# Optimization experiments

Measured on AMD Instinct MI355X. Metric: run time of the kernel, lower is better.

## Reference

```python
import jax, jax.numpy as jnp
import numpy as np

B, S, T, H, VS, VE = 32, 128, 128, 512, 8000, 8000


def _lstm_scan(x_proj, W_hh, bias, h0, c0):
    # x_proj: [L, B, 4H] precomputed input projections; gate order i,f,g,o (PyTorch)
    def step(carry, xp):
        h, c = carry
        gates = xp + h @ W_hh.T + bias  # [B, 4H]
        i, f, g, o = jnp.split(gates, 4, axis=-1)
        c = jax.nn.sigmoid(f) * c + jax.nn.sigmoid(i) * jnp.tanh(g)
        h = jax.nn.sigmoid(o) * jnp.tanh(c)
        return (h, c), h
    (h, c), hs = jax.lax.scan(step, (h0, c0), x_proj)
    return hs, h, c


def setup_inputs() -> dict:
    key = jax.random.key(0)
    ks = jax.random.split(key, 16)
    sc_h = 1.0 / np.sqrt(H)
    u = lambda k, shape: jax.random.uniform(k, shape, jnp.float32, -sc_h, sc_h)
    return {
        "input_batch": jax.random.randint(ks[0], (B, S), 0, VS),
        "output_batch": jax.random.randint(ks[1], (B, T), 0, VE),
        "Wa": u(ks[2], (H, H)), "ba": u(ks[3], (H,)),
        "W1": u(ks[4], (H, 2 * H)), "b1": u(ks[5], (H,)),
        "W2": u(ks[6], (VE, H)), "b2": u(ks[7], (VE,)),
        "We_ih": u(ks[8], (4 * H, VS)), "We_hh": u(ks[9], (4 * H, H)),
        "be_ih": u(ks[10], (4 * H,)), "be_hh": u(ks[11], (4 * H,)),
        "Wd_ih": u(ks[12], (4 * H, VE)), "Wd_hh": u(ks[13], (4 * H, H)),
        "bd_ih": u(ks[14], (4 * H,)), "bd_hh": u(ks[15], (4 * H,)),
    }


def reference(input_batch, output_batch, Wa, ba, W1, b1, W2, b2,
              We_ih, We_hh, be_ih, be_hh, Wd_ih, Wd_hh, bd_ih, bd_hh):
    src = input_batch.T  # [S, B]
    tgt = output_batch.T  # [T, B]
    # one_hot(tok) @ W_ih.T  ==  W_ih.T[tok]  (gather instead of dense one-hot GEMM)
    enc_xp = jnp.take(We_ih.T, src, axis=0)  # [S, B, 4H]
    dec_xp = jnp.take(Wd_ih.T, tgt, axis=0)  # [T, B, 4H]
    h0 = jnp.zeros((B, H), jnp.float32)
    c0 = jnp.zeros((B, H), jnp.float32)
    enc_outputs, h, c = _lstm_scan(enc_xp, We_hh, be_ih + be_hh, h0, c0)  # [S,B,H]
    proj_enc = enc_outputs @ Wa.T + ba  # attn(enc_outputs): [S, B, H]
    dec_bias = bd_ih + bd_hh

    def dec_step(carry, xp):
        h, c = carry
        gates = xp + h @ Wd_hh.T + dec_bias
        i, f, g, o = jnp.split(gates, 4, axis=-1)
        c = jax.nn.sigmoid(f) * c + jax.nn.sigmoid(i) * jnp.tanh(g)
        h = jax.nn.sigmoid(o) * jnp.tanh(c)  # [B, H] == dec_output
        scores = jnp.einsum('sbh,bh->bs', proj_enc, h)  # [B, S]
        w = jax.nn.softmax(scores, axis=1)
        context = jnp.einsum('bs,sbh->bh', w, enc_outputs)  # [B, H]
        hid = jnp.tanh(jnp.concatenate([h, context], axis=1) @ W1.T + b1)
        logits = hid @ W2.T + b2  # [B, VE]
        return (h, c), logits

    _, model = jax.lax.scan(dec_step, (h, c), dec_xp)  # [T, B, VE]
    return jax.nn.softmax(model.transpose(1, 0, 2), axis=2)  # [B, T, VE]
```

## Files before the change

### kernel.cpp

```cpp
#include <hip/hip_runtime.h>
#include <hip/hip_cooperative_groups.h>

#define NB 32
#define NS 128
#define NT 128
#define NH 512
#define NVS 8000
#define NVE 8000

typedef float fx4 __attribute__((ext_vector_type(4)));

__device__ __forceinline__ float sigm(float x) { return 1.0f / (1.0f + expf(-x)); }

__device__ __forceinline__ fx4 load_cg(const float* p) {
  fx4 v;
  asm volatile("global_load_dwordx4 %0, %1, off sc0 sc1" : "=v"(v) : "v"(p));
  return v;
}
__device__ __forceinline__ void store_cg(float* p, fx4 v) {
  asm volatile("global_store_dwordx4 %0, %1, off sc0 sc1" :: "v"(p), "v"(v) : "memory");
}

__global__ __launch_bounds__(256) void scan_kernel(
    const int* __restrict__ in_tok, const int* __restrict__ out_tok,
    const float* __restrict__ We_ih, const float* __restrict__ We_hh,
    const float* __restrict__ be_ih, const float* __restrict__ be_hh,
    const float* __restrict__ Wd_ih, const float* __restrict__ Wd_hh,
    const float* __restrict__ bd_ih, const float* __restrict__ bd_hh,
    float* __restrict__ h_buf,
    float* __restrict__ enc_out,
    float* __restrict__ dec_h,
    int* __restrict__ flags)
{
  __shared__ float W_lds[16][520];
  __shared__ float h_lds[16 * 516];
  __shared__ float gbuf[16][16];
  __shared__ float c_buf[4][16];
  __shared__ float hstage[16][4];

  const int tid = threadIdx.x;
  const int g   = blockIdx.x;
  const int bg  = g & 1;
  const int mg  = g >> 1;
  const int r   = tid >> 4;
  const int bl  = tid & 15;
  const int b   = bg * 16 + bl;
  const int q   = r >> 2;
  const int i   = r & 3;
  const int j   = q * NH + mg * 4 + i;

  const float bias_e = be_ih[j] + be_hh[j];
  const float bias_d = bd_ih[j] + bd_hh[j];
  const float* Wcol_e = We_ih + (size_t)j * NVS;
  const float* Wcol_d = Wd_ih + (size_t)j * NVE;

  if (tid < 64) c_buf[tid >> 4][tid & 15] = 0.0f;

  {
    const float* Wg = We_hh;
    for (int u = tid; u < 2048; u += 256) {
      const int rr = u >> 7;
      const int k4 = (u & 127) << 2;
      const int jj = (rr >> 2) * NH + mg * 4 + (rr & 3);
      *(float4*)&W_lds[rr][k4] = *(const float4*)(Wg + (size_t)jj * NH + k4);
    }
  }
  __syncthreads();

  for (int s = 0; s < NS + NT; ++s) {
    const bool enc = (s < NS);
    if (s == NS) {
      const float* Wg = Wd_hh;
      for (int u = tid; u < 2048; u += 256) {
        const int rr = u >> 7;
        const int k4 = (u & 127) << 2;
        const int jj = (rr >> 2) * NH + mg * 4 + (rr & 3);
        *(float4*)&W_lds[rr][k4] = *(const float4*)(Wg + (size_t)jj * NH + k4);
      }
      __syncthreads();
    }
    const int st  = enc ? s : s - NS;
    const int tok = enc ? in_tok[b * NS + st] : out_tok[b * NT + st];
    const float xp = enc ? Wcol_e[tok] : Wcol_d[tok];
    const float bias = enc ? bias_e : bias_d;
    const float* Wrow = &W_lds[r][0];

    float acc = 0.0f;
    if (s > 0) {
      if (tid < 128) {
        const int idx = (tid << 1) | bg;
        while (__hip_atomic_load(&flags[idx], __ATOMIC_RELAXED,
                                 __HIP_MEMORY_SCOPE_AGENT) < s)
          __builtin_amdgcn_s_sleep(1);
      }
      __syncthreads();
      const float* hsrc = h_buf + ((s - 1) & 1) * (NB * NH) + bg * 16 * NH;
      fx4 tmp[8];
      #pragma unroll
      for (int it = 0; it < 8; ++it)
        tmp[it] = load_cg(hsrc + ((tid + (it << 8)) << 2));
      asm volatile("s_waitcnt vmcnt(0)" ::: "memory");
      __builtin_amdgcn_sched_barrier(0);
      #pragma unroll
      for (int it = 0; it < 8; ++it) {
        const int u = tid + (it << 8);
        const int bb = u >> 7;
        const int kk = (u & 127) << 2;
        *(fx4*)&h_lds[bb * 516 + kk] = tmp[it];
      }
      __syncthreads();
      const float* hrow = &h_lds[bl * 516];
      #pragma unroll 8
      for (int k = 0; k < NH; k += 4) {
        const float4 hv = *(const float4*)(hrow + k);
        const float4 wv = *(const float4*)(Wrow + k);
        acc += hv.x * wv.x + hv.y * wv.y + hv.z * wv.z + hv.w * wv.w;
      }
    }
    gbuf[r][bl] = acc + xp + bias;
    __syncthreads();

    if (tid < 64) {
      const int ii = tid >> 4;
      const int bb = tid & 15;
      const float gi = gbuf[ii][bb];
      const float gf = gbuf[4 + ii][bb];
      const float gg = gbuf[8 + ii][bb];
      const float go = gbuf[12 + ii][bb];
      const float co = c_buf[ii][bb];
      const float cn = sigm(gf) * co + sigm(gi) * tanhf(gg);
      const float hn = sigm(go) * tanhf(cn);
      c_buf[ii][bb] = cn;
      hstage[bb][ii] = hn;
    }
    __syncthreads();
    if (tid < 16) {
      const fx4 hv = *(const fx4*)&hstage[tid][0];
      const int bglob = bg * 16 + tid;
      store_cg(h_buf + (s & 1) * (NB * NH) + bglob * NH + mg * 4, hv);
      float* dst = enc ? (enc_out + ((size_t)st * NB + bglob) * NH + mg * 4)
                       : (dec_h  + ((size_t)st * NB + bglob) * NH + mg * 4);
      *(fx4*)dst = hv;
    }
    asm volatile("s_waitcnt vmcnt(0)" ::: "memory");
    __syncthreads();
    if (tid == 0)
      __hip_atomic_store(&flags[g], s + 1, __ATOMIC_RELAXED,
                         __HIP_MEMORY_SCOPE_AGENT);
  }
}

template<int TRANSB, int CSWAP, int ACT>
__global__ __launch_bounds__(256) void gemm64(
    const float* __restrict__ A, const float* __restrict__ Bm,
    float* __restrict__ C, const float* __restrict__ bias,
    const float* __restrict__ A2, int ksplit,
    int M, int N, int K, int lda, int ldb, int ldc,
    long batchA, long batchB, long batchC)
{
  __shared__ float As[16][68];
  __shared__ float Bs[16][68];
  const int z = blockIdx.z;
  A += (long)z * batchA;
  if (A2 != nullptr) A2 += (long)z * batchA;
  Bm += (long)z * batchB;
  C  += (long)z * batchC;
  const int m0 = blockIdx.y << 6;
  const int n0 = blockIdx.x << 6;
  const int tid = threadIdx.x;
  const int tx = tid & 15;
  const int ty = tid >> 4;
  float acc[4][4] = {};

  for (int k0 = 0; k0 < K; k0 += 16) {
    {
      const int mrow = tid >> 2;
      const int kcq = (tid & 3) << 2;
      const float* base = A;
      int keff = k0;
      if (A2 != nullptr && k0 >= ksplit) { base = A2; keff = k0 - ksplit; }
      const float4 v = *(const float4*)(base + (long)(m0 + mrow) * lda + keff + kcq);
      As[kcq + 0][mrow] = v.x; As[kcq + 1][mrow] = v.y;
      As[kcq + 2][mrow] = v.z; As[kcq + 3][mrow] = v.w;
    }
    if (TRANSB == 0) {
      const int nrow = tid >> 2;
      const int kcq = (tid & 3) << 2;
      const float4 v = *(const float4*)(Bm + (long)(n0 + nrow) * ldb + k0 + kcq);
      Bs[kcq + 0][nrow] = v.x; Bs[kcq + 1][nrow] = v.y;
      Bs[kcq + 2][nrow] = v.z; Bs[kcq + 3][nrow] = v.w;
    } else {
      const int krow = tid >> 4;
      const int nc = (tid & 15) << 2;
      const float4 v = *(const float4*)(Bm + (long)(k0 + krow) * ldb + n0 + nc);
      *(float4*)&Bs[krow][nc] = v;
    }
    __syncthreads();
    #pragma unroll
    for (int kk = 0; kk < 16; ++kk) {
      const float4 a4 = *(const float4*)&As[kk][ty << 2];
      const float4 b4 = *(const float4*)&Bs[kk][tx << 2];
      const float a[4]  = {a4.x, a4.y, a4.z, a4.w};
      const float bv[4] = {b4.x, b4.y, b4.z, b4.w};
      #pragma unroll
      for (int ii = 0; ii < 4; ++ii)
        #pragma unroll
        for (int jj = 0; jj < 4; ++jj)
          acc[ii][jj] = fmaf(a[ii], bv[jj], acc[ii][jj]);
    }
    __syncthreads();
  }

  const int n = n0 + (tx << 2);
  float4 bb4 = {0.f, 0.f, 0.f, 0.f};
  if (bias) { bb4.x = bias[n]; bb4.y = bias[n + 1]; bb4.z = bias[n + 2]; bb4.w = bias[n + 3]; }
  #pragma unroll
  for (int ii = 0; ii < 4; ++ii) {
    const int mrow = m0 + (ty << 2) + ii;
    float4 o;
    o.x = acc[ii][0] + bb4.x; o.y = acc[ii][1] + bb4.y;
    o.z = acc[ii][2] + bb4.z; o.w = acc[ii][3] + bb4.w;
    if (ACT == 1) { o.x = tanhf(o.x); o.y = tanhf(o.y); o.z = tanhf(o.z); o.w = tanhf(o.w); }
    long orow = mrow;
    if (CSWAP) orow = (long)(mrow & (NB - 1)) * NT + (mrow >> 5);
    *(float4*)(C + orow * (long)ldc + n) = o;
  }
}

template<int CSWAP, int ACT>
__global__ __launch_bounds__(256) void gemm128(
    const float* __restrict__ A, const float* __restrict__ Bm,
    float* __restrict__ C, const float* __restrict__ bias,
    const float* __restrict__ A2, int ksplit,
    int M, int N, int K, int lda, int ldb, int ldc)
{
  __shared__ float As[16][132];
  __shared__ float Bs[16][68];
  const int m0 = blockIdx.y << 7;
  const int n0 = blockIdx.x << 6;
  const int tid = threadIdx.x;
  const int tx = tid & 15;
  const int ty = tid >> 4;
  float acc[8][4] = {};

  for (int k0 = 0; k0 < K; k0 += 16) {
    {
      const int mrow = tid >> 1;
      const int kq = (tid & 1) << 3;
      const float* base = A;
      int keff = k0;
      if (A2 != nullptr && k0 >= ksplit) { base = A2; keff = k0 - ksplit; }
      const float* p = base + (long)(m0 + mrow) * lda + keff + kq;
      const float4 v0 = *(const float4*)(p);
      const float4 v1 = *(const float4*)(p + 4);
      As[kq + 0][mrow] = v0.x; As[kq + 1][mrow] = v0.y;
      As[kq + 2][mrow] = v0.z; As[kq + 3][mrow] = v0.w;
      As[kq + 4][mrow] = v1.x; As[kq + 5][mrow] = v1.y;
      As[kq + 6][mrow] = v1.z; As[kq + 7][mrow] = v1.w;
    }
    {
      const int nrow = tid >> 2;
      const int kq = (tid & 3) << 2;
      const float4 v = *(const float4*)(Bm + (long)(n0 + nrow) * ldb + k0 + kq);
      Bs[kq + 0][nrow] = v.x; Bs[kq + 1][nrow] = v.y;
      Bs[kq + 2][nrow] = v.z; Bs[kq + 3][nrow] = v.w;
    }
    __syncthreads();
    #pragma unroll
    for (int kk = 0; kk < 16; ++kk) {
      const fx4 b4 = *(const fx4*)&Bs[kk][tx << 2];
      const fx4 a0 = *(const fx4*)&As[kk][ty << 3];
      const fx4 a1 = *(const fx4*)&As[kk][(ty << 3) + 4];
      #pragma unroll
      for (int ii = 0; ii < 4; ++ii) {
        #pragma unroll
        for (int jj = 0; jj < 4; ++jj) {
          acc[ii][jj]     = fmaf(a0[ii], b4[jj], acc[ii][jj]);
          acc[ii + 4][jj] = fmaf(a1[ii], b4[jj], acc[ii + 4][jj]);
        }
      }
    }
    __syncthreads();
  }

  const int n = n0 + (tx << 2);
  float4 bb4 = {0.f, 0.f, 0.f, 0.f};
  if (bias) { bb4.x = bias[n]; bb4.y = bias[n + 1]; bb4.z = bias[n + 2]; bb4.w = bias[n + 3]; }
  #pragma unroll
  for (int ii = 0; ii < 8; ++ii) {
    const int mrow = m0 + (ty << 3) + ii;
    float4 o;
    o.x = acc[ii][0] + bb4.x; o.y = acc[ii][1] + bb4.y;
    o.z = acc[ii][2] + bb4.z; o.w = acc[ii][3] + bb4.w;
    if (ACT == 1) { o.x = tanhf(o.x); o.y = tanhf(o.y); o.z = tanhf(o.z); o.w = tanhf(o.w); }
    long orow = mrow;
    if (CSWAP) orow = (long)(mrow & (NB - 1)) * NT + (mrow >> 5);
    *(float4*)(C + orow * (long)ldc + n) = o;
  }
}

__global__ __launch_bounds__(128) void softmax_s(float* __restrict__ sc) {
  const long row = blockIdx.x;
  float* p = sc + row * NS;
  const float x = p[threadIdx.x];
  float mx = x;
  for (int o = 32; o; o >>= 1) mx = fmaxf(mx, __shfl_xor(mx, o));
  __shared__ float r0[2], r1[2];
  const int w = threadIdx.x >> 6;
  if ((threadIdx.x & 63) == 0) r0[w] = mx;
  __syncthreads();
  mx = fmaxf(r0[0], r0[1]);
  const float e = expf(x - mx);
  float sum = e;
  for (int o = 32; o; o >>= 1) sum += __shfl_xor(sum, o);
  if ((threadIdx.x & 63) == 0) r1[w] = sum;
  __syncthreads();
  sum = r1[0] + r1[1];
  p[threadIdx.x] = e / sum;
}

__global__ __launch_bounds__(256) void softmax_v(float* __restrict__ out) {
  const long row = blockIdx.x;
  float* p = out + row * NVE;
  float v[32];
  float mx = -1e30f;
  #pragma unroll
  for (int it = 0; it < 32; ++it) {
    const int idx = (it << 8) + threadIdx.x;
    v[it] = (idx < NVE) ? p[idx] : -1e30f;
    mx = fmaxf(mx, v[it]);
  }
  for (int o = 32; o; o >>= 1) mx = fmaxf(mx, __shfl_xor(mx, o));
  __shared__ float red[4], red2[4];
  const int w = threadIdx.x >> 6;
  if ((threadIdx.x & 63) == 0) red[w] = mx;
  __syncthreads();
  mx = fmaxf(fmaxf(red[0], red[1]), fmaxf(red[2], red[3]));
  float sum = 0.0f;
  #pragma unroll
  for (int it = 0; it < 32; ++it) {
    const int idx = (it << 8) + threadIdx.x;
    if (idx < NVE) { v[it] = expf(v[it] - mx); sum += v[it]; }
  }
  for (int o = 32; o; o >>= 1) sum += __shfl_xor(sum, o);
  if ((threadIdx.x & 63) == 0) red2[w] = sum;
  __syncthreads();
  sum = red2[0] + red2[1] + red2[2] + red2[3];
  const float inv = 1.0f / sum;
  #pragma unroll
  for (int it = 0; it < 32; ++it) {
    const int idx = (it << 8) + threadIdx.x;
    if (idx < NVE) p[idx] = v[it] * inv;
  }
}

extern "C" void kernel_launch(void* const* d_in, const int* in_sizes, int n_in,
                              void* d_out, int out_size, void* d_ws, size_t ws_size,
                              hipStream_t stream) {
  const int*   in_tok = (const int*)d_in[0];
  const int*   out_tok = (const int*)d_in[1];
  const float* Wa    = (const float*)d_in[2];
  const float* ba    = (const float*)d_in[3];
  const float* W1    = (const float*)d_in[4];
  const float* b1    = (const float*)d_in[5];
  const float* W2    = (const float*)d_in[6];
  const float* b2    = (const float*)d_in[7];
  const float* We_ih = (const float*)d_in[8];
  const float* We_hh = (const float*)d_in[9];
  const float* be_ih = (const float*)d_in[10];
  const float* be_hh = (const float*)d_in[11];
  const float* Wd_ih = (const float*)d_in[12];
  const float* Wd_hh = (const float*)d_in[13];
  const float* bd_ih = (const float*)d_in[14];
  const float* bd_hh = (const float*)d_in[15];

  float* ws      = (float*)d_ws;
  float* h_buf   = ws;
  float* enc_out = ws + 32768;
  float* dec_h   = ws + 2129920;
  float* proj    = ws + 4227072;
  float* scores  = ws + 6324224;
  float* ctx     = ws + 6848512;
  float* hid     = ws + 8945664;
  int*   flags   = (int*)(ws + 11042816);
  float* out     = (float*)d_out;

  (void)hipMemsetAsync((void*)flags, 0, 256 * sizeof(int), stream);

  {
    void* args[14];
    args[0] = (void*)&in_tok; args[1] = (void*)&out_tok;
    args[2] = (void*)&We_ih;  args[3] = (void*)&We_hh;
    args[4] = (void*)&be_ih;  args[5] = (void*)&be_hh;
    args[6] = (void*)&Wd_ih;  args[7] = (void*)&Wd_hh;
    args[8] = (void*)&bd_ih;  args[9] = (void*)&bd_hh;
    args[10] = (void*)&h_buf; args[11] = (void*)&enc_out; args[12] = (void*)&dec_h;
    args[13] = (void*)&flags;
    (void)hipLaunchCooperativeKernel((void*)scan_kernel, dim3(256), dim3(256), args, 0, stream);
  }

  gemm128<0,0><<<dim3(8,32,1), 256, 0, stream>>>(
      enc_out, Wa, proj, ba, nullptr, 1 << 30,
      4096, 512, 512, 512, 512, 512);

  gemm64<0,0,0><<<dim3(2,2,NB), 256, 0, stream>>>(
      dec_h, proj, scores, nullptr, nullptr, 1 << 30,
      NT, NS, NH, NB * NH, NB * NH, NB * NS,
      (long)NH, (long)NH, (long)NS);

  softmax_s<<<dim3(NT * NB), 128, 0, stream>>>(scores);

  gemm64<1,0,0><<<dim3(8,2,NB), 256, 0, stream>>>(
      scores, enc_out, ctx, nullptr, nullptr, 1 << 30,
      NT, NH, NS, NB * NS, NB * NH, NB * NH,
      (long)NS, (long)NH, (long)NH);

  gemm128<0,1><<<dim3(8,32,1), 256, 0, stream>>>(
      dec_h, W1, hid, b1, ctx, 512,
      4096, 512, 1024, 512, 1024, 512);

  gemm128<1,0><<<dim3(125,32,1), 256, 0, stream>>>(
      hid, W2, out, b2, nullptr, 1 << 30,
      4096, NVE, 512, 512, 512, NVE);

  softmax_v<<<dim3(NB * NT), 256, 0, stream>>>(out);
}
```

Measured before the change: 2.240 ms.

## Decentralize scan flag polling per thread and use taller tile GEMM for vocab projection

In the recurrent scan kernel, each thread now polls only the producer flag for the slice of h it loads. This replaces the block-wide poll-then-barrier. The h-publish path uses wave shuffles instead of an LDS staging buffer, and the flag is set as soon as the h_buf store completes, before the enc_out/dec_h store, which shortens the serial critical path per timestep. Separately, the output vocab GEMM switches to a new 256x64-tile kernel to raise per-thread register reuse, at the cost of more registers and fewer blocks.

Measured after the change: 2.915 ms. 30.1% more time.

```diff
diff --git a/kernel.cpp b/kernel.cpp
--- a/kernel.cpp
+++ b/kernel.cpp
@@ -36,7 +36,6 @@
   __shared__ float h_lds[16 * 516];
   __shared__ float gbuf[16][16];
   __shared__ float c_buf[4][16];
-  __shared__ float hstage[16][4];
 
   const int tid = threadIdx.x;
   const int g   = blockIdx.x;
@@ -49,6 +48,10 @@
   const int i   = r & 3;
   const int j   = q * NH + mg * 4 + i;
 
+  const int gp  = tid >> 1;
+  const int hb  = tid & 1;
+  const int pflag = gp * 2 + bg;
+
   const float bias_e = be_ih[j] + be_hh[j];
   const float bias_d = bd_ih[j] + bd_hh[j];
   const float* Wcol_e = We_ih + (size_t)j * NVS;
@@ -56,26 +59,22 @@
 
   if (tid < 64) c_buf[tid >> 4][tid & 15] = 0.0f;
 
-  {
-    const float* Wg = We_hh;
-    for (int u = tid; u < 2048; u += 256) {
-      const int rr = u >> 7;
-      const int k4 = (u & 127) << 2;
-      const int jj = (rr >> 2) * NH + mg * 4 + (rr & 3);
-      *(float4*)&W_lds[rr][k4] = *(const float4*)(Wg + (size_t)jj * NH + k4);
-    }
+  for (int u = tid; u < 2048; u += 256) {
+    const int rr = u >> 7;
+    const int k4 = (u & 127) << 2;
+    const int jj = (rr >> 2) * NH + mg * 4 + (rr & 3);
+    *(float4*)&W_lds[rr][k4] = *(const float4*)(We_hh + (size_t)jj * NH + k4);
   }
   __syncthreads();
 
   for (int s = 0; s < NS + NT; ++s) {
     const bool enc = (s < NS);
     if (s == NS) {
-      const float* Wg = Wd_hh;
       for (int u = tid; u < 2048; u += 256) {
         const int rr = u >> 7;
         const int k4 = (u & 127) << 2;
         const int jj = (rr >> 2) * NH + mg * 4 + (rr & 3);
-        *(float4*)&W_lds[rr][k4] = *(const float4*)(Wg + (size_t)jj * NH + k4);
+        *(float4*)&W_lds[rr][k4] = *(const float4*)(Wd_hh + (size_t)jj * NH + k4);
       }
       __syncthreads();
     }
@@ -87,27 +86,19 @@
 
     float acc = 0.0f;
     if (s > 0) {
-      if (tid < 128) {
-        const int idx = (tid << 1) | bg;
-        while (__hip_atomic_load(&flags[idx], __ATOMIC_RELAXED,
-                                 __HIP_MEMORY_SCOPE_AGENT) < s)
-          __builtin_amdgcn_s_sleep(1);
-      }
-      __syncthreads();
+      while (__hip_atomic_load(&flags[pflag], __ATOMIC_RELAXED,
+                               __HIP_MEMORY_SCOPE_AGENT) < s)
+        __builtin_amdgcn_s_sleep(1);
       const float* hsrc = h_buf + ((s - 1) & 1) * (NB * NH) + bg * 16 * NH;
-      fx4 tmp[8];
-      #pragma unroll
-      for (int it = 0; it < 8; ++it)
-        tmp[it] = load_cg(hsrc + ((tid + (it << 8)) << 2));
+      fx4 t[8];
+      #pragma unroll
+      for (int u = 0; u < 8; ++u)
+        t[u] = load_cg(hsrc + (hb * 8 + u) * NH + gp * 4);
       asm volatile("s_waitcnt vmcnt(0)" ::: "memory");
       __builtin_amdgcn_sched_barrier(0);
       #pragma unroll
-      for (int it = 0; it < 8; ++it) {
-        const int u = tid + (it << 8);
-        const int bb = u >> 7;
-        const int kk = (u & 127) << 2;
-        *(fx4*)&h_lds[bb * 516 + kk] = tmp[it];
-      }
+      for (int u = 0; u < 8; ++u)
+        *(fx4*)&h_lds[(hb * 8 + u) * 516 + gp * 4] = t[u];
       __syncthreads();
       const float* hrow = &h_lds[bl * 516];
       #pragma unroll 8
@@ -131,22 +122,27 @@
       const float cn = sigm(gf) * co + sigm(gi) * tanhf(gg);
       const float hn = sigm(go) * tanhf(cn);
       c_buf[ii][bb] = cn;
-      hstage[bb][ii] = hn;
-    }
-    __syncthreads();
-    if (tid < 16) {
-      const fx4 hv = *(const fx4*)&hstage[tid][0];
-      const int bglob = bg * 16 + tid;
-      store_cg(h_buf + (s & 1) * (NB * NH) + bglob * NH + mg * 4, hv);
-      float* dst = enc ? (enc_out + ((size_t)st * NB + bglob) * NH + mg * 4)
-                       : (dec_h  + ((size_t)st * NB + bglob) * NH + mg * 4);
-      *(fx4*)dst = hv;
-    }
-    asm volatile("s_waitcnt vmcnt(0)" ::: "memory");
-    __syncthreads();
-    if (tid == 0)
-      __hip_atomic_store(&flags[g], s + 1, __ATOMIC_RELAXED,
-                         __HIP_MEMORY_SCOPE_AGENT);
+      const int lb = tid & 15;
+      fx4 hv;
+      hv.x = __shfl(hn, lb);
+      hv.y = __shfl(hn, lb + 16);
+      hv.z = __shfl(hn, lb + 32);
+      hv.w = __shfl(hn, lb + 48);
+      if (tid < 16) {
+        const int bglob = bg * 16 + tid;
+        store_cg(h_buf + (s & 1) * (NB * NH) + bglob * NH + mg * 4, hv);
+      }
+      asm volatile("s_waitcnt vmcnt(0)" ::: "memory");
+      if (tid == 0)
+        __hip_atomic_store(&flags[g], s + 1, __ATOMIC_RELAXED,
+                           __HIP_MEMORY_SCOPE_AGENT);
+      if (tid < 16) {
+        const int bglob = bg * 16 + tid;
+        float* dst = enc ? (enc_out + ((size_t)st * NB + bglob) * NH + mg * 4)
+                         : (dec_h  + ((size_t)st * NB + bglob) * NH + mg * 4);
+        *(fx4*)dst = hv;
+      }
+    }
   }
 }
 
@@ -299,6 +295,71 @@
   }
 }
 
+template<int CSWAP, int ACT>
+__global__ __launch_bounds__(256) void gemm256(
+    const float* __restrict__ A, const float* __restrict__ Bm,
+    float* __restrict__ C, const float* __restrict__ bias,
+    int M, int N, int K, int lda, int ldb, int ldc)
+{
+  __shared__ float As[16][260];
+  __shared__ float Bs[16][68];
+  const int m0 = blockIdx.y << 8;
+  const int n0 = blockIdx.x << 6;
+  const int tid = threadIdx.x;
+  const int tx = tid & 15;
+  const int ty = tid >> 4;
+  float acc[16][4] = {};
+
+  for (int k0 = 0; k0 < K; k0 += 16) {
+    {
+      const float* p = A + (long)(m0 + tid) * lda + k0;
+      #pragma unroll
+      for (int u = 0; u < 4; ++u) {
+        const float4 v = *(const float4*)(p + (u << 2));
+        As[(u << 2) + 0][tid] = v.x; As[(u << 2) + 1][tid] = v.y;
+        As[(u << 2) + 2][tid] = v.z; As[(u << 2) + 3][tid] = v.w;
+      }
+    }
+    {
+      const int nrow = tid >> 2;
+      const int kq = (tid & 3) << 2;
+      const float4 v = *(const float4*)(Bm + (long)(n0 + nrow) * ldb + k0 + kq);
+      Bs[kq + 0][nrow] = v.x; Bs[kq + 1][nrow] = v.y;
+      Bs[kq + 2][nrow] = v.z; Bs[kq + 3][nrow] = v.w;
+    }
+    __syncthreads();
+    #pragma unroll
+    for (int kk = 0; kk < 16; ++kk) {
+      const fx4 b4 = *(const fx4*)&Bs[kk][tx << 2];
+      #pragma unroll
+      for (int gq = 0; gq < 4; ++gq) {
+        const fx4 a4 = *(const fx4*)&As[kk][(ty << 4) + (gq << 2)];
+        #pragma unroll
+        for (int ii = 0; ii < 4; ++ii)
+          #pragma unroll
+          for (int jj = 0; jj < 4; ++jj)
+            acc[(gq << 2) + ii][jj] = fmaf(a4[ii], b4[jj], acc[(gq << 2) + ii][jj]);
+      }
+    }
+    __syncthreads();
+  }
+
+  const int n = n0 + (tx << 2);
+  float4 bb4 = {0.f, 0.f, 0.f, 0.f};
+  if (bias) { bb4.x = bias[n]; bb4.y = bias[n + 1]; bb4.z = bias[n + 2]; bb4.w = bias[n + 3]; }
+  #pragma unroll
+  for (int ii = 0; ii < 16; ++ii) {
+    const int mrow = m0 + (ty << 4) + ii;
+    float4 o;
+    o.x = acc[ii][0] + bb4.x; o.y = acc[ii][1] + bb4.y;
+    o.z = acc[ii][2] + bb4.z; o.w = acc[ii][3] + bb4.w;
+    if (ACT == 1) { o.x = tanhf(o.x); o.y = tanhf(o.y); o.z = tanhf(o.z); o.w = tanhf(o.w); }
+    long orow = mrow;
+    if (CSWAP) orow = (long)(mrow & (NB - 1)) * NT + (mrow >> 5);
+    *(float4*)(C + orow * (long)ldc + n) = o;
+  }
+}
+
 __global__ __launch_bounds__(128) void softmax_s(float* __restrict__ sc) {
   const long row = blockIdx.x;
   float* p = sc + row * NS;
@@ -419,8 +480,8 @@
       dec_h, W1, hid, b1, ctx, 512,
       4096, 512, 1024, 512, 1024, 512);
 
-  gemm128<1,0><<<dim3(125,32,1), 256, 0, stream>>>(
-      hid, W2, out, b2, nullptr, 1 << 30,
+  gemm256<1,0><<<dim3(125,16,1), 256, 0, stream>>>(
+      hid, W2, out, b2,
       4096, NVE, 512, 512, 512, NVE);
 
   softmax_v<<<dim3(NB * NT), 256, 0, stream>>>(out);
```

## Shorten per-step barrier chain in persistent LSTM scan with shuffles and per-thread polling

Applied to the files above, without the earlier changes.

Every thread now polls its own producer flag instead of 128 threads polling followed by a block barrier. The gathered hidden state is built with wavefront shuffles rather than an LDS staging buffer and an extra __syncthreads. The flag is published before the enc_out/dec_h store so consumers are released sooner. The aim is to cut serial synchronisation latency on each of the 256 dependent steps. The trade-off is more threads spinning on atomics and reliance on in-wave ordering between the c_buf write and the next step.

Measured after the change: 2.894 ms. +29.2%, slower.

```diff
diff --git a/kernel.cpp b/kernel.cpp
--- a/kernel.cpp
+++ b/kernel.cpp
@@ -36,7 +36,6 @@
   __shared__ float h_lds[16 * 516];
   __shared__ float gbuf[16][16];
   __shared__ float c_buf[4][16];
-  __shared__ float hstage[16][4];
 
   const int tid = threadIdx.x;
   const int g   = blockIdx.x;
@@ -49,6 +48,8 @@
   const int i   = r & 3;
   const int j   = q * NH + mg * 4 + i;
 
+  const int pflag = ((tid & 127) << 1) | bg;
+
   const float bias_e = be_ih[j] + be_hh[j];
   const float bias_d = bd_ih[j] + bd_hh[j];
   const float* Wcol_e = We_ih + (size_t)j * NVS;
@@ -56,26 +57,22 @@
 
   if (tid < 64) c_buf[tid >> 4][tid & 15] = 0.0f;
 
-  {
-    const float* Wg = We_hh;
-    for (int u = tid; u < 2048; u += 256) {
-      const int rr = u >> 7;
-      const int k4 = (u & 127) << 2;
-      const int jj = (rr >> 2) * NH + mg * 4 + (rr & 3);
-      *(float4*)&W_lds[rr][k4] = *(const float4*)(Wg + (size_t)jj * NH + k4);
-    }
+  for (int u = tid; u < 2048; u += 256) {
+    const int rr = u >> 7;
+    const int k4 = (u & 127) << 2;
+    const int jj = (rr >> 2) * NH + mg * 4 + (rr & 3);
+    *(float4*)&W_lds[rr][k4] = *(const float4*)(We_hh + (size_t)jj * NH + k4);
   }
   __syncthreads();
 
   for (int s = 0; s < NS + NT; ++s) {
     const bool enc = (s < NS);
     if (s == NS) {
-      const float* Wg = Wd_hh;
       for (int u = tid; u < 2048; u += 256) {
         const int rr = u >> 7;
         const int k4 = (u & 127) << 2;
         const int jj = (rr >> 2) * NH + mg * 4 + (rr & 3);
-        *(float4*)&W_lds[rr][k4] = *(const float4*)(Wg + (size_t)jj * NH + k4);
+        *(float4*)&W_lds[rr][k4] = *(const float4*)(Wd_hh + (size_t)jj * NH + k4);
       }
       __syncthreads();
     }
@@ -87,18 +84,14 @@
 
     float acc = 0.0f;
     if (s > 0) {
-      if (tid < 128) {
-        const int idx = (tid << 1) | bg;
-        while (__hip_atomic_load(&flags[idx], __ATOMIC_RELAXED,
-                                 __HIP_MEMORY_SCOPE_AGENT) < s)
-          __builtin_amdgcn_s_sleep(1);
-      }
-      __syncthreads();
+      while (__hip_atomic_load(&flags[pflag], __ATOMIC_RELAXED,
+                               __HIP_MEMORY_SCOPE_AGENT) < s)
+        __builtin_amdgcn_s_sleep(1);
       const float* hsrc = h_buf + ((s - 1) & 1) * (NB * NH) + bg * 16 * NH;
-      fx4 tmp[8];
+      fx4 t[8];
       #pragma unroll
       for (int it = 0; it < 8; ++it)
-        tmp[it] = load_cg(hsrc + ((tid + (it << 8)) << 2));
+        t[it] = load_cg(hsrc + ((tid + (it << 8)) << 2));
       asm volatile("s_waitcnt vmcnt(0)" ::: "memory");
       __builtin_amdgcn_sched_barrier(0);
       #pragma unroll
@@ -106,7 +99,7 @@
         const int u = tid + (it << 8);
         const int bb = u >> 7;
         const int kk = (u & 127) << 2;
-        *(fx4*)&h_lds[bb * 516 + kk] = tmp[it];
+        *(fx4*)&h_lds[bb * 516 + kk] = t[it];
       }
       __syncthreads();
       const float* hrow = &h_lds[bl * 516];
@@ -131,22 +124,27 @@
       const float cn = sigm(gf) * co + sigm(gi) * tanhf(gg);
       const float hn = sigm(go) * tanhf(cn);
       c_buf[ii][bb] = cn;
-      hstage[bb][ii] = hn;
-    }
-    __syncthreads();
-    if (tid < 16) {
-      const fx4 hv = *(const fx4*)&hstage[tid][0];
-      const int bglob = bg * 16 + tid;
-      store_cg(h_buf + (s & 1) * (NB * NH) + bglob * NH + mg * 4, hv);
-      float* dst = enc ? (enc_out + ((size_t)st * NB + bglob) * NH + mg * 4)
-                       : (dec_h  + ((size_t)st * NB + bglob) * NH + mg * 4);
-      *(fx4*)dst = hv;
-    }
-    asm volatile("s_waitcnt vmcnt(0)" ::: "memory");
-    __syncthreads();
-    if (tid == 0)
-      __hip_atomic_store(&flags[g], s + 1, __ATOMIC_RELAXED,
-                         __HIP_MEMORY_SCOPE_AGENT);
+      const int lb = tid & 15;
+      fx4 hv;
+      hv.x = __shfl(hn, lb);
+      hv.y = __shfl(hn, lb + 16);
+      hv.z = __shfl(hn, lb + 32);
+      hv.w = __shfl(hn, lb + 48);
+      if (tid < 16) {
+        const int bglob = bg * 16 + tid;
+        store_cg(h_buf + (s & 1) * (NB * NH) + bglob * NH + mg * 4, hv);
+      }
+      asm volatile("s_waitcnt vmcnt(0)" ::: "memory");
+      if (tid == 0)
+        __hip_atomic_store(&flags[g], s + 1, __ATOMIC_RELAXED,
+                           __HIP_MEMORY_SCOPE_AGENT);
+      if (tid < 16) {
+        const int bglob = bg * 16 + tid;
+        float* dst = enc ? (enc_out + ((size_t)st * NB + bglob) * NH + mg * 4)
+                         : (dec_h  + ((size_t)st * NB + bglob) * NH + mg * 4);
+        *(fx4*)dst = hv;
+      }
+    }
   }
 }
 
```
